# Optimization experiments

Hardware: AMD Instinct MI355X
Metric: run time of the kernel (lower is better)

The kernel has to match this reference:

```python
import jax, jax.numpy as jnp
import numpy as np

N_AGT, N_CTX, E, D = 100000, 150000, 500000, 128
EPS = 1e-5


def gn(x, g, b):
    # GroupNorm(1, C) on [N, C] == per-row layernorm over channels
    mu = jnp.mean(x, axis=-1, keepdims=True)
    var = jnp.mean((x - mu) ** 2, axis=-1, keepdims=True)
    return (x - mu) * jax.lax.rsqrt(var + EPS) * g + b


def setup_inputs() -> dict:
    key = jax.random.key(0)
    ks = jax.random.split(key, 24)
    def w(k, i, o):
        return jax.random.normal(k, (i, o), jnp.float32) * (1.0 / np.sqrt(i))
    inp = {
        "agts": jax.random.normal(ks[0], (N_AGT, D), jnp.float32),
        "ctx": jax.random.normal(ks[1], (N_CTX, D), jnp.float32),
        "agt_ctrs": jax.random.normal(ks[2], (N_AGT, 2), jnp.float32),
        "ctx_ctrs": jax.random.normal(ks[3], (N_CTX, 2), jnp.float32),
        # dist MLP: Linear(2,128,bias) -> ReLU -> Linear(128,128,no bias) -> GN -> ReLU
        "W_dist1": w(ks[4], 2, D), "b_dist1": jnp.zeros((D,), jnp.float32),
        "W_dist2": w(ks[5], D, D), "g_dist": jnp.ones((D,), jnp.float32), "b_dist": jnp.zeros((D,), jnp.float32),
        # query: Linear(128,128,no bias) -> GN -> ReLU
        "W_q": w(ks[6], D, D), "g_q": jnp.ones((D,), jnp.float32), "b_q": jnp.zeros((D,), jnp.float32),
        # ctx MLP: Linear(384,128,no bias)->GN->ReLU -> Linear(128,128,no bias)
        "W_c1": w(ks[7], 3 * D, D), "g_c1": jnp.ones((D,), jnp.float32), "b_c1": jnp.zeros((D,), jnp.float32),
        "W_c2": w(ks[8], D, D),
        # agt: Linear(128,128,no bias)
        "W_agt": w(ks[9], D, D),
        # norm after scatter
        "g_n": jnp.ones((D,), jnp.float32), "b_n": jnp.zeros((D,), jnp.float32),
        # linear: Linear(128,128,no bias)->GN (no act)
        "W_lin": w(ks[10], D, D), "g_lin": jnp.ones((D,), jnp.float32), "b_lin": jnp.zeros((D,), jnp.float32),
        # precomputed edge lists (dist<=100 mask in the original)
        "hi": jax.random.randint(ks[11], (E,), 0, N_AGT, jnp.int32),
        "wi": jax.random.randint(ks[12], (E,), 0, N_CTX, jnp.int32),
    }
    return inp


def reference(agts, ctx, agt_ctrs, ctx_ctrs,
              W_dist1, b_dist1, W_dist2, g_dist, b_dist,
              W_q, g_q, b_q,
              W_c1, g_c1, b_c1, W_c2,
              W_agt, g_n, b_n,
              W_lin, g_lin, b_lin,
              hi, wi):
    res = agts
    # gather + dist MLP
    d = agt_ctrs[hi] - ctx_ctrs[wi]                    # [E, 2]
    d = jax.nn.relu(d @ W_dist1 + b_dist1)             # [E, D]
    d = jax.nn.relu(gn(d @ W_dist2, g_dist, b_dist))
    # query from gathered agent features
    q = jax.nn.relu(gn(agts[hi] @ W_q, g_q, b_q))      # [E, D]
    # context message MLP
    c = jnp.concatenate([d, q, ctx[wi]], axis=1)       # [E, 3D]
    c = jax.nn.relu(gn(c @ W_c1, g_c1, b_c1))
    c = c @ W_c2                                       # [E, D]
    # scatter back, norm, residual
    a = agts @ W_agt                                   # [N_agt, D]
    a = a.at[hi].add(c)
    a = jax.nn.relu(gn(a, g_n, b_n))
    a = gn(a @ W_lin, g_lin, b_lin)
    a = jax.nn.relu(a + res)
    return a
```

## Files before the change

### kernel.cpp

```cpp
#include <hip/hip_runtime.h>
#include <math.h>

#define DD 128
#define CAP 32
constexpr float EPS = 1e-5f;

typedef __bf16 bf16x8 __attribute__((ext_vector_type(8)));
typedef float  f32x4  __attribute__((ext_vector_type(4)));

__device__ __forceinline__ float4 ld4(const float* p){ return *(const float4*)p; }

__device__ __forceinline__ bf16x8 cvt8(const float* p){
  bf16x8 r;
#pragma unroll
  for (int i=0;i<8;i++) r[i] = (__bf16)p[i];
  return r;
}

__global__ __launch_bounds__(256)
void pack_w(const float* W0, const float* W1, const float* W2, const float* W3,
            const float* W4, const float* W5, const float* W6, const float* W7,
            __bf16* dst){
  int gidx = blockIdx.x*256 + threadIdx.x;
  int mat  = gidx >> 11;
  int i    = gidx & 2047;
  int lane = i & 63, frag = i >> 6;
  int tn = frag >> 2, ks = frag & 3;
  int n  = tn*16 + (lane & 15);
  int k0 = ks*32 + (lane >> 4)*8;
  const float* W;
  switch(mat){
    case 0: W=W0; break; case 1: W=W1; break; case 2: W=W2; break; case 3: W=W3; break;
    case 4: W=W4; break; case 5: W=W5; break; case 6: W=W6; break; default: W=W7; break;
  }
  __bf16* d = dst + (size_t)mat*16384 + (size_t)i*8;
#pragma unroll
  for (int j=0;j<8;j++) d[j] = (__bf16)W[(size_t)(k0+j)*DD + n];
}

template<bool RELU>
__device__ __forceinline__ void gn_frag(f32x4 (&acc)[8], const float* __restrict__ g,
                                        const float* __restrict__ b, int m){
  float gv[8], bv[8];
#pragma unroll
  for (int t=0;t<8;t++){ gv[t]=g[t*16+m]; bv[t]=b[t*16+m]; }
#pragma unroll
  for (int r=0;r<4;r++){
    float s=0.f, sq=0.f;
#pragma unroll
    for (int t=0;t<8;t++){ float v=acc[t][r]; s+=v; sq=fmaf(v,v,sq); }
#pragma unroll
    for (int mk=1; mk<16; mk<<=1){ s+=__shfl_xor(s,mk,64); sq+=__shfl_xor(sq,mk,64); }
    float mu=s*(1.f/DD);
    float rs=rsqrtf(sq*(1.f/DD)-mu*mu+EPS);
#pragma unroll
    for (int t=0;t<8;t++){
      float v=(acc[t][r]-mu)*rs*gv[t]+bv[t];
      if (RELU) v=fmaxf(v,0.f);
      acc[t][r]=v;
    }
  }
}

__device__ __forceinline__ void mfma_all(const bf16x8 (&af)[4], const __bf16* __restrict__ Wp,
                                         f32x4 (&acc)[8], int lane){
#pragma unroll
  for (int tn=0;tn<8;tn++){
    f32x4 a; a[0]=0.f; a[1]=0.f; a[2]=0.f; a[3]=0.f;
#pragma unroll
    for (int ks=0;ks<4;ks++){
      bf16x8 bf = *(const bf16x8*)(Wp + ((size_t)((tn*4+ks)*64 + lane))*8);
      a = __builtin_amdgcn_mfma_f32_16x16x32_bf16(af[ks], bf, a, 0,0,0);
    }
    acc[tn]=a;
  }
}

__device__ __forceinline__ void read_af(const __bf16* T, bf16x8 (&af)[4], int w, int lane){
  int m=lane&15, q=lane>>4;
#pragma unroll
  for (int ks=0;ks<4;ks++)
    af[ks] = *(const bf16x8*)(T + (16*w+m)*136 + ks*32 + q*8);
}

__device__ __forceinline__ void write_cfrag_bf16(__bf16* T, const f32x4 (&acc)[8], int w, int lane){
  int m=lane&15, q=lane>>4;
#pragma unroll
  for (int r=0;r<4;r++){
    int row=16*w+4*q+r;
#pragma unroll
    for (int t=0;t<8;t++) T[row*136 + t*16 + m] = (__bf16)acc[t][r];
  }
}

__device__ __forceinline__ void load_af_f32(const float* X, bf16x8 (&af)[4], int row, int M, int q){
  if (row < M){
    const float* xr = X + (size_t)row*DD;
#pragma unroll
    for (int ks=0;ks<4;ks++){
      float t[8];
      *(float4*)t     = ld4(xr + ks*32 + q*8);
      *(float4*)(t+4) = ld4(xr + ks*32 + q*8 + 4);
      af[ks] = cvt8(t);
    }
  } else {
#pragma unroll
    for (int ks=0;ks<4;ks++){
#pragma unroll
      for (int j=0;j<8;j++) af[ks][j]=(__bf16)0.f;
    }
  }
}

__global__ __launch_bounds__(256)
void prep_kernel(const int* __restrict__ hi, int E, int* __restrict__ counts, int* __restrict__ perm,
                 const float* __restrict__ agts,
                 const __bf16* __restrict__ Wp_q, const float* __restrict__ g_q, const float* __restrict__ b_q,
                 const __bf16* __restrict__ Wp_mid, const __bf16* __restrict__ Wp_agt,
                 __bf16* __restrict__ Aq2bf, float* __restrict__ baseF, int nA,
                 const float* __restrict__ ctx, const __bf16* __restrict__ Wp_chi,
                 __bf16* __restrict__ Ccbf, int nC,
                 int gBucket, int gA){
  __shared__ __bf16 T[64*136];
  int b = blockIdx.x;
  if (b < gBucket){
    int e = b*256 + threadIdx.x;
    if (e < E){
      int a = hi[e];
      int slot = atomicAdd(&counts[a], 1);
      if (slot < CAP) perm[(size_t)a*CAP + slot] = e;
    }
    return;
  }
  b -= gBucket;
  int tid=threadIdx.x, w=tid>>6, lane=tid&63, m=lane&15, q=lane>>4;
  if (b < gA){
    int rowA = b*64 + 16*w + m;
    bf16x8 af_a[4];
    load_af_f32(agts, af_a, rowA, nA, q);
    f32x4 acc[8];
    mfma_all(af_a, Wp_q, acc, lane);
    gn_frag<true>(acc, g_q, b_q, m);
    write_cfrag_bf16(T, acc, w, lane);
    bf16x8 af_q[4];
    read_af(T, af_q, w, lane);
    mfma_all(af_q, Wp_mid, acc, lane);
#pragma unroll
    for (int r=0;r<4;r++){
      int row = b*64 + 16*w + 4*q + r;
      if (row < nA){
#pragma unroll
        for (int t=0;t<8;t++)
          Aq2bf[(size_t)row*DD + t*16 + m] = (__bf16)acc[t][r];
      }
    }
    if (baseF){
      mfma_all(af_a, Wp_agt, acc, lane);
#pragma unroll
      for (int r=0;r<4;r++){
        int row = b*64 + 16*w + 4*q + r;
        if (row < nA){
#pragma unroll
          for (int t=0;t<8;t++)
            baseF[(size_t)row*DD + t*16 + m] = acc[t][r];
        }
      }
    }
  } else {
    int bid = b - gA;
    int rowA = bid*64 + 16*w + m;
    bf16x8 af[4];
    load_af_f32(ctx, af, rowA, nC, q);
    f32x4 acc[8];
    mfma_all(af, Wp_chi, acc, lane);
#pragma unroll
    for (int r=0;r<4;r++){
      int row = bid*64 + 16*w + 4*q + r;
      if (row < nC){
#pragma unroll
        for (int t=0;t<8;t++)
          Ccbf[(size_t)row*DD + t*16 + m] = (__bf16)acc[t][r];
      }
    }
  }
}

__global__ __launch_bounds__(256)
void edge_kernel(const float* __restrict__ agt_ctrs, const float* __restrict__ ctx_ctrs,
                 const int* __restrict__ hi, const int* __restrict__ wi,
                 const float* __restrict__ W1, const float* __restrict__ B1,
                 const __bf16* __restrict__ Wp_d2, const float* __restrict__ g_dist, const float* __restrict__ b_dist,
                 const __bf16* __restrict__ Wp_c1, const float* __restrict__ g_c1, const float* __restrict__ b_c1,
                 const __bf16* __restrict__ Wp_c2,
                 const __bf16* __restrict__ Aq2, const __bf16* __restrict__ Cc,
                 float* __restrict__ accOut, __bf16* __restrict__ edge_out, int E){
  __shared__ __bf16 T[64*136];
  int tid=threadIdx.x, w=tid>>6, lane=tid&63, m=lane&15, q=lane>>4;
  int eBase = blockIdx.x*64;
  int grow = tid>>2, gch = tid&3;
  int ge = eBase + grow;
  int ghe=0, gwe=0;
  if (ge < E){ ghe = hi[ge]; gwe = wi[ge]; }
  bf16x8 ga[4], gc[4];
  {
    const __bf16* ap = Aq2 + (size_t)ghe*DD + gch*32;
    const __bf16* cp = Cc  + (size_t)gwe*DD + gch*32;
#pragma unroll
    for (int c2=0;c2<4;c2++){ ga[c2]=*(const bf16x8*)(ap+c2*8); gc[c2]=*(const bf16x8*)(cp+c2*8); }
  }
  {
    int e0 = lane, e = eBase + e0;
    float dx=0.f, dy=0.f;
    if (e < E){
      int h0=hi[e], w0=wi[e];
      dx = agt_ctrs[2*h0]   - ctx_ctrs[2*w0];
      dy = agt_ctrs[2*h0+1] - ctx_ctrs[2*w0+1];
    }
#pragma unroll
    for (int s=0;s<4;s++){
      float t[8];
#pragma unroll
      for (int j=0;j<8;j++){
        int c = w*32 + s*8 + j;
        t[j] = fmaxf(fmaf(dx, W1[c], fmaf(dy, W1[DD+c], B1[c])), 0.f);
      }
      *(bf16x8*)(T + e0*136 + w*32 + s*8) = cvt8(t);
    }
  }
  __syncthreads();
  bf16x8 af[4]; f32x4 acc[8];
  read_af(T, af, w, lane);
  mfma_all(af, Wp_d2, acc, lane);
  gn_frag<true>(acc, g_dist, b_dist, m);
  write_cfrag_bf16(T, acc, w, lane);
  read_af(T, af, w, lane);
#pragma unroll
  for (int c2=0;c2<4;c2++){
    float s[8];
#pragma unroll
    for (int j=0;j<8;j++) s[j] = (float)ga[c2][j] + (float)gc[c2][j];
    *(bf16x8*)(T + grow*136 + gch*32 + c2*8) = cvt8(s);
  }
  mfma_all(af, Wp_c1, acc, lane);
#pragma unroll
  for (int r=0;r<4;r++){
    int row = 16*w + 4*q + r;
#pragma unroll
    for (int t=0;t<8;t++)
      acc[t][r] += (float)T[row*136 + t*16 + m];
  }
  gn_frag<true>(acc, g_c1, b_c1, m);
  write_cfrag_bf16(T, acc, w, lane);
  read_af(T, af, w, lane);
  mfma_all(af, Wp_c2, acc, lane);
  if (edge_out){
    write_cfrag_bf16(T, acc, w, lane);
    if (ge < E){
      const __bf16* src = T + grow*136 + gch*32;
      __bf16* dst = edge_out + (size_t)ge*DD + gch*32;
#pragma unroll
      for (int c2=0;c2<4;c2++) *(bf16x8*)(dst + c2*8) = *(const bf16x8*)(src + c2*8);
    }
  } else {
#pragma unroll
    for (int r=0;r<4;r++){
      int row = 16*w + 4*q + r;
      if (eBase + row < E){
        int he = hi[eBase + row];
        float* dst = accOut + (size_t)he*DD + m;
#pragma unroll
        for (int t=0;t<8;t++)
          atomicAdd(dst + t*16, acc[t][r]);
      }
    }
  }
}

__global__ __launch_bounds__(256)
void final_fused(const float* __restrict__ agts, const __bf16* __restrict__ Wp_agt,
                 const int* __restrict__ counts, const int* __restrict__ perm,
                 const __bf16* __restrict__ edge_out,
                 const float* __restrict__ g_n, const float* __restrict__ b_n,
                 const __bf16* __restrict__ Wp_lin, const float* __restrict__ g_lin, const float* __restrict__ b_lin,
                 float* __restrict__ out, int M){
  __shared__ float Tf[64*132];
  __shared__ __bf16 T[64*136];
  int tid=threadIdx.x, w=tid>>6, lane=tid&63, m=lane&15, q=lane>>4;
  int rowBase=blockIdx.x*64;
  bf16x8 af_a[4];
  load_af_f32(agts, af_a, rowBase + 16*w + m, M, q);
  f32x4 acc[8];
  mfma_all(af_a, Wp_agt, acc, lane);
#pragma unroll
  for (int r=0;r<4;r++){
    int row=16*w+4*q+r;
#pragma unroll
    for (int t=0;t<8;t++) Tf[row*132 + t*16 + m] = acc[t][r];
  }
  int grow=tid>>2, gch=tid&3;
  int a = rowBase + grow;
  float s[32];
#pragma unroll
  for (int c2=0;c2<8;c2++){
    float4 v = *(const float4*)(Tf + grow*132 + gch*32 + c2*4);
    s[c2*4]=v.x; s[c2*4+1]=v.y; s[c2*4+2]=v.z; s[c2*4+3]=v.w;
  }
  int cnt = 0;
  if (a < M){ cnt = counts[a]; cnt = cnt < CAP ? cnt : CAP; }
  for (int j=0;j<cnt;j++){
    int e = perm[(size_t)a*CAP + j];
    const __bf16* ep = edge_out + (size_t)e*DD + gch*32;
#pragma unroll
    for (int c2=0;c2<4;c2++){
      bf16x8 v = *(const bf16x8*)(ep + c2*8);
#pragma unroll
      for (int k=0;k<8;k++) s[c2*8+k] += (float)v[k];
    }
  }
  {
    float sm=0.f, sq=0.f;
#pragma unroll
    for (int k=0;k<32;k++){ sm+=s[k]; sq=fmaf(s[k],s[k],sq); }
    sm+=__shfl_xor(sm,1,64); sm+=__shfl_xor(sm,2,64);
    sq+=__shfl_xor(sq,1,64); sq+=__shfl_xor(sq,2,64);
    float mu=sm*(1.f/DD), rs=rsqrtf(sq*(1.f/DD)-mu*mu+EPS);
#pragma unroll
    for (int k=0;k<32;k++){
      int c=gch*32+k;
      s[k]=fmaxf((s[k]-mu)*rs*g_n[c]+b_n[c],0.f);
    }
  }
#pragma unroll
  for (int c2=0;c2<4;c2++)
    *(bf16x8*)(T + grow*136 + gch*32 + c2*8) = cvt8(s + c2*8);
  bf16x8 af[4];
  read_af(T, af, w, lane);
  mfma_all(af, Wp_lin, acc, lane);
  gn_frag<false>(acc, g_lin, b_lin, m);
#pragma unroll
  for (int r=0;r<4;r++){
    int row=rowBase+16*w+4*q+r;
    if (row<M){
#pragma unroll
      for (int t=0;t<8;t++){
        int col=t*16+m;
        float rr=agts[(size_t)row*DD+col];
        out[(size_t)row*DD+col]=fmaxf(acc[t][r]+rr,0.f);
      }
    }
  }
}

__global__ __launch_bounds__(256)
void final_kernel(const float* __restrict__ accF, const float* __restrict__ g_n, const float* __restrict__ b_n,
                  const __bf16* __restrict__ Wp_lin, const float* __restrict__ g_lin, const float* __restrict__ b_lin,
                  const float* __restrict__ res, float* __restrict__ out, int M){
  __shared__ __bf16 Ab[64*136];
  int tid=threadIdx.x, w=tid>>6, lane=tid&63, m=lane&15, q=lane>>4;
  int rowBase=blockIdx.x*64;
  {
    int rl=tid>>2, qq=tid&3;
    int row=rowBase+rl;
    float v[32];
    float s=0.f, sq=0.f;
#pragma unroll
    for (int t8=0;t8<8;t8++){
      float4 x=make_float4(0.f,0.f,0.f,0.f);
      if (row<M) x=ld4(accF + (size_t)row*DD + qq*32 + t8*4);
      v[t8*4]=x.x; v[t8*4+1]=x.y; v[t8*4+2]=x.z; v[t8*4+3]=x.w;
      s  += x.x+x.y+x.z+x.w;
      sq += x.x*x.x+x.y*x.y+x.z*x.z+x.w*x.w;
    }
    s+=__shfl_xor(s,1,64); s+=__shfl_xor(s,2,64);
    sq+=__shfl_xor(sq,1,64); sq+=__shfl_xor(sq,2,64);
    float mu=s*(1.f/DD), rs=rsqrtf(sq*(1.f/DD)-mu*mu+EPS);
#pragma unroll
    for (int j=0;j<32;j++){
      int c=qq*32+j;
      v[j]=fmaxf((v[j]-mu)*rs*g_n[c]+b_n[c],0.f);
    }
#pragma unroll
    for (int s2=0;s2<4;s2++)
      *(bf16x8*)(Ab + rl*136 + qq*32 + s2*8) = cvt8(v+s2*8);
  }
  __syncthreads();
  bf16x8 af[4]; f32x4 acc[8];
  read_af(Ab, af, w, lane);
  mfma_all(af, Wp_lin, acc, lane);
  gn_frag<false>(acc, g_lin, b_lin, m);
#pragma unroll
  for (int r=0;r<4;r++){
    int row=rowBase+16*w+4*q+r;
    if (row<M){
#pragma unroll
      for (int t=0;t<8;t++){
        int col=t*16+m;
        float rr=res[(size_t)row*DD+col];
        out[(size_t)row*DD+col]=fmaxf(acc[t][r]+rr,0.f);
      }
    }
  }
}

extern "C" void kernel_launch(void* const* d_in, const int* in_sizes, int n_in,
                              void* d_out, int out_size, void* d_ws, size_t ws_size,
                              hipStream_t stream){
  const float* agts     = (const float*)d_in[0];
  const float* ctx      = (const float*)d_in[1];
  const float* agt_ctrs = (const float*)d_in[2];
  const float* ctx_ctrs = (const float*)d_in[3];
  const float* W_dist1  = (const float*)d_in[4];
  const float* b_dist1  = (const float*)d_in[5];
  const float* W_dist2  = (const float*)d_in[6];
  const float* g_dist   = (const float*)d_in[7];
  const float* b_dist   = (const float*)d_in[8];
  const float* W_q      = (const float*)d_in[9];
  const float* g_q      = (const float*)d_in[10];
  const float* b_q      = (const float*)d_in[11];
  const float* W_c1     = (const float*)d_in[12];
  const float* g_c1     = (const float*)d_in[13];
  const float* b_c1     = (const float*)d_in[14];
  const float* W_c2     = (const float*)d_in[15];
  const float* W_agt    = (const float*)d_in[16];
  const float* g_n      = (const float*)d_in[17];
  const float* b_n      = (const float*)d_in[18];
  const float* W_lin    = (const float*)d_in[19];
  const float* g_lin    = (const float*)d_in[20];
  const float* b_lin    = (const float*)d_in[21];
  const int*   hi       = (const int*)d_in[22];
  const int*   wi       = (const int*)d_in[23];

  int nA = in_sizes[0]/DD, nC = in_sizes[1]/DD, nE = in_sizes[22];
  float* out = (float*)d_out;

  auto al = [](size_t x){ return (x + 255) & ~(size_t)255; };
  size_t oAq2 = 0;
  size_t oCc  = al(oAq2 + (size_t)nA*DD*2);
  size_t oWp  = al(oCc  + (size_t)nC*DD*2);
  size_t oCnt = al(oWp  + (size_t)8*16384*2);
  size_t oPerm= al(oCnt + (size_t)nA*4);
  size_t oTail= al(oPerm+ (size_t)nA*CAP*4);
  size_t needA = oTail + (size_t)nE*DD*2;
  bool bigA = (ws_size >= needA);

  char* ws = (char*)d_ws;
  __bf16* Aq2bf = (__bf16*)(ws + oAq2);
  __bf16* Ccbf  = (__bf16*)(ws + oCc);
  __bf16* Wp    = (__bf16*)(ws + oWp);
  int*    counts= (int*)   (ws + oCnt);
  int*    perm  = (int*)   (ws + oPerm);
  __bf16* edge_out = (__bf16*)(ws + oTail);
  float*  CF    = (float*)(ws + oCnt);

  dim3 B(256);
  int gA=(nA+63)/64, gC=(nC+63)/64, gE=(nE+63)/64;
  int gBucket = bigA ? (nE+255)/256 : 0;

  pack_w<<<64,B,0,stream>>>(W_dist2, W_c1, W_c2, W_q,
                            W_c1+128*DD, W_c1+256*DD, W_agt, W_lin, Wp);
  if (bigA){
    hipMemsetAsync(counts, 0, (size_t)nA*4, stream);
    prep_kernel<<<gBucket+gA+gC,B,0,stream>>>(hi, nE, counts, perm,
        agts, Wp+3*16384, g_q, b_q, Wp+4*16384, Wp+6*16384, Aq2bf, nullptr, nA,
        ctx, Wp+5*16384, Ccbf, nC, gBucket, gA);
    edge_kernel<<<gE,B,0,stream>>>(agt_ctrs, ctx_ctrs, hi, wi,
        W_dist1, b_dist1, Wp+0, g_dist, b_dist,
        Wp+1*16384, g_c1, b_c1, Wp+2*16384,
        Aq2bf, Ccbf, nullptr, edge_out, nE);
    final_fused<<<gA,B,0,stream>>>(agts, Wp+6*16384, counts, perm, edge_out,
        g_n, b_n, Wp+7*16384, g_lin, b_lin, out, nA);
  } else {
    prep_kernel<<<gA+gC,B,0,stream>>>(hi, nE, counts, perm,
        agts, Wp+3*16384, g_q, b_q, Wp+4*16384, Wp+6*16384, Aq2bf, CF, nA,
        ctx, Wp+5*16384, Ccbf, nC, 0, gA);
    edge_kernel<<<gE,B,0,stream>>>(agt_ctrs, ctx_ctrs, hi, wi,
        W_dist1, b_dist1, Wp+0, g_dist, b_dist,
        Wp+1*16384, g_c1, b_c1, Wp+2*16384,
        Aq2bf, Ccbf, CF, nullptr, nE);
    final_kernel<<<gA,B,0,stream>>>(CF, g_n, b_n, Wp+7*16384, g_lin, b_lin, agts, out, nA);
  }
}
```

Baseline: 540.2 us.

## Permute weight columns so MFMA outputs are contiguous, enabling vector stores

Packs weight columns in a permuted order so each lane's eight MFMA output tiles map to eight contiguous columns. Scalar strided global and LDS stores become 16-byte vector stores, and gamma/beta/residual loads become float4s. The edge kernel now writes its output straight from registers, and one __syncthreads is dropped because each wave now builds only its own rows. The scatter kernel's fp32 staging tile is replaced by a bf16 one, which lowers LDS use but rounds the base activations to bf16.

```diff
diff --git a/kernel.cpp b/kernel.cpp
--- a/kernel.cpp
+++ b/kernel.cpp
@@ -26,7 +26,7 @@
   int i    = gidx & 2047;
   int lane = i & 63, frag = i >> 6;
   int tn = frag >> 2, ks = frag & 3;
-  int n  = tn*16 + (lane & 15);
+  int n  = (lane & 15)*8 + tn;
   int k0 = ks*32 + (lane >> 4)*8;
   const float* W;
   switch(mat){
@@ -42,8 +42,8 @@
 __device__ __forceinline__ void gn_frag(f32x4 (&acc)[8], const float* __restrict__ g,
                                         const float* __restrict__ b, int m){
   float gv[8], bv[8];
-#pragma unroll
-  for (int t=0;t<8;t++){ gv[t]=g[t*16+m]; bv[t]=b[t*16+m]; }
+  *(float4*)gv     = ld4(g + m*8); *(float4*)(gv+4) = ld4(g + m*8 + 4);
+  *(float4*)bv     = ld4(b + m*8); *(float4*)(bv+4) = ld4(b + m*8 + 4);
 #pragma unroll
   for (int r=0;r<4;r++){
     float s=0.f, sq=0.f;
@@ -88,8 +88,38 @@
 #pragma unroll
   for (int r=0;r<4;r++){
     int row=16*w+4*q+r;
-#pragma unroll
-    for (int t=0;t<8;t++) T[row*136 + t*16 + m] = (__bf16)acc[t][r];
+    bf16x8 v;
+#pragma unroll
+    for (int t=0;t<8;t++) v[t]=(__bf16)acc[t][r];
+    *(bf16x8*)(T + row*136 + m*8) = v;
+  }
+}
+
+__device__ __forceinline__ void st_c_bf16(__bf16* Y, const f32x4 (&acc)[8], int rowBase,
+                                          int w, int q, int m, int M){
+#pragma unroll
+  for (int r=0;r<4;r++){
+    int row = rowBase + 16*w + 4*q + r;
+    if (row < M){
+      bf16x8 v;
+#pragma unroll
+      for (int t=0;t<8;t++) v[t]=(__bf16)acc[t][r];
+      *(bf16x8*)(Y + (size_t)row*DD + m*8) = v;
+    }
+  }
+}
+
+__device__ __forceinline__ void st_c_f32(float* Y, const f32x4 (&acc)[8], int rowBase,
+                                         int w, int q, int m, int M){
+#pragma unroll
+  for (int r=0;r<4;r++){
+    int row = rowBase + 16*w + 4*q + r;
+    if (row < M){
+      float4 a0 = make_float4(acc[0][r],acc[1][r],acc[2][r],acc[3][r]);
+      float4 a1 = make_float4(acc[4][r],acc[5][r],acc[6][r],acc[7][r]);
+      *(float4*)(Y + (size_t)row*DD + m*8)     = a0;
+      *(float4*)(Y + (size_t)row*DD + m*8 + 4) = a1;
+    }
   }
 }
 
@@ -145,43 +175,18 @@
     bf16x8 af_q[4];
     read_af(T, af_q, w, lane);
     mfma_all(af_q, Wp_mid, acc, lane);
-#pragma unroll
-    for (int r=0;r<4;r++){
-      int row = b*64 + 16*w + 4*q + r;
-      if (row < nA){
-#pragma unroll
-        for (int t=0;t<8;t++)
-          Aq2bf[(size_t)row*DD + t*16 + m] = (__bf16)acc[t][r];
-      }
-    }
+    st_c_bf16(Aq2bf, acc, b*64, w, q, m, nA);
     if (baseF){
       mfma_all(af_a, Wp_agt, acc, lane);
-#pragma unroll
-      for (int r=0;r<4;r++){
-        int row = b*64 + 16*w + 4*q + r;
-        if (row < nA){
-#pragma unroll
-          for (int t=0;t<8;t++)
-            baseF[(size_t)row*DD + t*16 + m] = acc[t][r];
-        }
-      }
+      st_c_f32(baseF, acc, b*64, w, q, m, nA);
     }
   } else {
     int bid = b - gA;
-    int rowA = bid*64 + 16*w + m;
     bf16x8 af[4];
-    load_af_f32(ctx, af, rowA, nC, q);
+    load_af_f32(ctx, af, bid*64 + 16*w + m, nC, q);
     f32x4 acc[8];
     mfma_all(af, Wp_chi, acc, lane);
-#pragma unroll
-    for (int r=0;r<4;r++){
-      int row = bid*64 + 16*w + 4*q + r;
-      if (row < nC){
-#pragma unroll
-        for (int t=0;t<8;t++)
-          Ccbf[(size_t)row*DD + t*16 + m] = (__bf16)acc[t][r];
-      }
-    }
+    st_c_bf16(Ccbf, acc, bid*64, w, q, m, nC);
   }
 }
 
@@ -209,7 +214,8 @@
     for (int c2=0;c2<4;c2++){ ga[c2]=*(const bf16x8*)(ap+c2*8); gc[c2]=*(const bf16x8*)(cp+c2*8); }
   }
   {
-    int e0 = lane, e = eBase + e0;
+    int er = m;
+    int e = eBase + 16*w + er;
     float dx=0.f, dy=0.f;
     if (e < E){
       int h0=hi[e], w0=wi[e];
@@ -218,16 +224,17 @@
     }
 #pragma unroll
     for (int s=0;s<4;s++){
-      float t[8];
-#pragma unroll
-      for (int j=0;j<8;j++){
-        int c = w*32 + s*8 + j;
-        t[j] = fmaxf(fmaf(dx, W1[c], fmaf(dy, W1[DD+c], B1[c])), 0.f);
-      }
-      *(bf16x8*)(T + e0*136 + w*32 + s*8) = cvt8(t);
-    }
-  }
-  __syncthreads();
+      int c0 = q*32 + s*8;
+      float wa[8], wb[8], bb[8], t[8];
+      *(float4*)wa = ld4(W1+c0);    *(float4*)(wa+4) = ld4(W1+c0+4);
+      *(float4*)wb = ld4(W1+DD+c0); *(float4*)(wb+4) = ld4(W1+DD+c0+4);
+      *(float4*)bb = ld4(B1+c0);    *(float4*)(bb+4) = ld4(B1+c0+4);
+#pragma unroll
+      for (int j=0;j<8;j++)
+        t[j] = fmaxf(fmaf(dx, wa[j], fmaf(dy, wb[j], bb[j])), 0.f);
+      *(bf16x8*)(T + (16*w+er)*136 + c0) = cvt8(t);
+    }
+  }
   bf16x8 af[4]; f32x4 acc[8];
   read_af(T, af, w, lane);
   mfma_all(af, Wp_d2, acc, lane);
@@ -245,21 +252,24 @@
 #pragma unroll
   for (int r=0;r<4;r++){
     int row = 16*w + 4*q + r;
-#pragma unroll
-    for (int t=0;t<8;t++)
-      acc[t][r] += (float)T[row*136 + t*16 + m];
+    bf16x8 tv = *(const bf16x8*)(T + row*136 + m*8);
+#pragma unroll
+    for (int t=0;t<8;t++) acc[t][r] += (float)tv[t];
   }
   gn_frag<true>(acc, g_c1, b_c1, m);
   write_cfrag_bf16(T, acc, w, lane);
   read_af(T, af, w, lane);
   mfma_all(af, Wp_c2, acc, lane);
   if (edge_out){
-    write_cfrag_bf16(T, acc, w, lane);
-    if (ge < E){
-      const __bf16* src = T + grow*136 + gch*32;
-      __bf16* dst = edge_out + (size_t)ge*DD + gch*32;
-#pragma unroll
-      for (int c2=0;c2<4;c2++) *(bf16x8*)(dst + c2*8) = *(const bf16x8*)(src + c2*8);
+#pragma unroll
+    for (int r=0;r<4;r++){
+      int erow = eBase + 16*w + 4*q + r;
+      if (erow < E){
+        bf16x8 v;
+#pragma unroll
+        for (int t=0;t<8;t++) v[t]=(__bf16)acc[t][r];
+        *(bf16x8*)(edge_out + (size_t)erow*DD + m*8) = v;
+      }
     }
   } else {
 #pragma unroll
@@ -267,10 +277,10 @@
       int row = 16*w + 4*q + r;
       if (eBase + row < E){
         int he = hi[eBase + row];
-        float* dst = accOut + (size_t)he*DD + m;
+        float* dst = accOut + (size_t)he*DD + m*8;
 #pragma unroll
         for (int t=0;t<8;t++)
-          atomicAdd(dst + t*16, acc[t][r]);
+          atomicAdd(dst + t, acc[t][r]);
       }
     }
   }
@@ -283,7 +293,6 @@
                  const float* __restrict__ g_n, const float* __restrict__ b_n,
                  const __bf16* __restrict__ Wp_lin, const float* __restrict__ g_lin, const float* __restrict__ b_lin,
                  float* __restrict__ out, int M){
-  __shared__ float Tf[64*132];
   __shared__ __bf16 T[64*136];
   int tid=threadIdx.x, w=tid>>6, lane=tid&63, m=lane&15, q=lane>>4;
   int rowBase=blockIdx.x*64;
@@ -291,19 +300,15 @@
   load_af_f32(agts, af_a, rowBase + 16*w + m, M, q);
   f32x4 acc[8];
   mfma_all(af_a, Wp_agt, acc, lane);
-#pragma unroll
-  for (int r=0;r<4;r++){
-    int row=16*w+4*q+r;
-#pragma unroll
-    for (int t=0;t<8;t++) Tf[row*132 + t*16 + m] = acc[t][r];
-  }
+  write_cfrag_bf16(T, acc, w, lane);
   int grow=tid>>2, gch=tid&3;
   int a = rowBase + grow;
   float s[32];
 #pragma unroll
-  for (int c2=0;c2<8;c2++){
-    float4 v = *(const float4*)(Tf + grow*132 + gch*32 + c2*4);
-    s[c2*4]=v.x; s[c2*4+1]=v.y; s[c2*4+2]=v.z; s[c2*4+3]=v.w;
+  for (int c2=0;c2<4;c2++){
+    bf16x8 bv = *(const bf16x8*)(T + grow*136 + gch*32 + c2*8);
+#pragma unroll
+    for (int k=0;k<8;k++) s[c2*8+k] = (float)bv[k];
   }
   int cnt = 0;
   if (a < M){ cnt = counts[a]; cnt = cnt < CAP ? cnt : CAP; }
@@ -324,11 +329,15 @@
     sm+=__shfl_xor(sm,1,64); sm+=__shfl_xor(sm,2,64);
     sq+=__shfl_xor(sq,1,64); sq+=__shfl_xor(sq,2,64);
     float mu=sm*(1.f/DD), rs=rsqrtf(sq*(1.f/DD)-mu*mu+EPS);
-#pragma unroll
-    for (int k=0;k<32;k++){
-      int c=gch*32+k;
-      s[k]=fmaxf((s[k]-mu)*rs*g_n[c]+b_n[c],0.f);
-    }
+    float gv[32], bv[32];
+#pragma unroll
+    for (int c2=0;c2<8;c2++){
+      *(float4*)(gv+c2*4) = ld4(g_n + gch*32 + c2*4);
+      *(float4*)(bv+c2*4) = ld4(b_n + gch*32 + c2*4);
+    }
+#pragma unroll
+    for (int k=0;k<32;k++)
+      s[k]=fmaxf((s[k]-mu)*rs*gv[k]+bv[k],0.f);
   }
 #pragma unroll
   for (int c2=0;c2<4;c2++)
@@ -341,12 +350,15 @@
   for (int r=0;r<4;r++){
     int row=rowBase+16*w+4*q+r;
     if (row<M){
-#pragma unroll
-      for (int t=0;t<8;t++){
-        int col=t*16+m;
-        float rr=agts[(size_t)row*DD+col];
-        out[(size_t)row*DD+col]=fmaxf(acc[t][r]+rr,0.f);
-      }
+      float rr[8];
+      *(float4*)rr     = ld4(agts + (size_t)row*DD + m*8);
+      *(float4*)(rr+4) = ld4(agts + (size_t)row*DD + m*8 + 4);
+      float4 o0 = make_float4(fmaxf(acc[0][r]+rr[0],0.f), fmaxf(acc[1][r]+rr[1],0.f),
+                              fmaxf(acc[2][r]+rr[2],0.f), fmaxf(acc[3][r]+rr[3],0.f));
+      float4 o1 = make_float4(fmaxf(acc[4][r]+rr[4],0.f), fmaxf(acc[5][r]+rr[5],0.f),
+                              fmaxf(acc[6][r]+rr[6],0.f), fmaxf(acc[7][r]+rr[7],0.f));
+      *(float4*)(out + (size_t)row*DD + m*8)     = o0;
+      *(float4*)(out + (size_t)row*DD + m*8 + 4) = o1;
     }
   }
 }
@@ -392,12 +404,15 @@
   for (int r=0;r<4;r++){
     int row=rowBase+16*w+4*q+r;
     if (row<M){
-#pragma unroll
-      for (int t=0;t<8;t++){
-        int col=t*16+m;
-        float rr=res[(size_t)row*DD+col];
-        out[(size_t)row*DD+col]=fmaxf(acc[t][r]+rr,0.f);
-      }
+      float rr[8];
+      *(float4*)rr     = ld4(res + (size_t)row*DD + m*8);
+      *(float4*)(rr+4) = ld4(res + (size_t)row*DD + m*8 + 4);
+      float4 o0 = make_float4(fmaxf(acc[0][r]+rr[0],0.f), fmaxf(acc[1][r]+rr[1],0.f),
+                              fmaxf(acc[2][r]+rr[2],0.f), fmaxf(acc[3][r]+rr[3],0.f));
+      float4 o1 = make_float4(fmaxf(acc[4][r]+rr[4],0.f), fmaxf(acc[5][r]+rr[5],0.f),
+                              fmaxf(acc[6][r]+rr[6],0.f), fmaxf(acc[7][r]+rr[7],0.f));
+      *(float4*)(out + (size_t)row*DD + m*8)     = o0;
+      *(float4*)(out + (size_t)row*DD + m*8 + 4) = o1;
     }
   }
 }
```

New measurement: 601.6 us. +11.4%, slower.
